# Kernel optimization log

Measured on AMD Instinct MI355X. Metric: run time of the kernel, lower is better.

The kernel has to match this reference:

```python
import jax, jax.numpy as jnp
import numpy as np

N, Fdim, Aout = 8192, 32, 8
AVG_DEG = 32.0  # target average degree for the random graph


def setup_inputs() -> dict:
    key = jax.random.key(0)
    ks = jax.random.split(key, 12)
    x = jax.random.normal(ks[0], (N, Fdim), dtype=jnp.float32)
    # binary adjacency, zero diagonal (GCNConv adds self-loops itself)
    u = jax.random.uniform(ks[1], (N, N), dtype=jnp.float32)
    adj = (u < (AVG_DEG / N)).astype(jnp.float32)
    adj = adj * (1.0 - jnp.eye(N, dtype=jnp.float32))
    mask = (jax.random.uniform(ks[2], (N,), dtype=jnp.float32) < 0.5).astype(jnp.float32)

    def lin(k, fout, fin):
        s = 1.0 / np.sqrt(fin)
        return jax.random.uniform(k, (fout, fin), jnp.float32, -s, s)

    return {
        "x": x, "adj": adj, "mask": mask,
        "w1": lin(ks[3], 64, Fdim), "b1": jnp.zeros((64,), jnp.float32),
        "w2": lin(ks[4], 128, 64), "b2": jnp.zeros((128,), jnp.float32),
        "wg": lin(ks[5], 128, 128), "bg": jnp.zeros((128,), jnp.float32),
        "wd": lin(ks[6], 128, 128), "bd": jnp.zeros((128,), jnp.float32),
        "wp1": lin(ks[7], 128, 256), "bp1": jnp.zeros((128,), jnp.float32),
        "wp2": lin(ks[8], 64, 128), "bp2": jnp.zeros((64,), jnp.float32),
        "wo": lin(ks[9], Aout, 64), "bo": jnp.zeros((Aout,), jnp.float32),
    }


def reference(x, adj, mask, w1, b1, w2, b2, wg, bg, wd, bd, wp1, bp1, wp2, bp2, wo, bo):
    # encoder MLP
    h = jax.nn.relu(x @ w1.T + b1)           # [N,64]
    h = jax.nn.relu(h @ w2.T + b2)           # [N,128]
    # GCNConv with default self-loops and symmetric normalization:
    # out = D^{-1/2} (A + I) D^{-1/2} (h W^T) + b
    a_hat = adj + jnp.eye(adj.shape[0], dtype=adj.dtype)
    deg = jnp.sum(a_hat, axis=1)             # >= 1 thanks to self-loops
    dinv = jax.lax.rsqrt(deg)
    msg = h @ wg.T                            # [N,128]
    agg = dinv[:, None] * (a_hat @ (dinv[:, None] * msg))  # normalized aggregation
    g = jax.nn.relu(agg + bg)
    g = jax.nn.relu(g @ wd.T + bd)
    f = jnp.concatenate([g, h], axis=1)       # [N,256]
    p = jax.nn.relu(f @ wp1.T + bp1)
    p = jax.nn.relu(p @ wp2.T + bp2)
    out = (p @ wo.T + bo) * mask[:, None]     # [N,Aout]
    return out
```

## Files before the change

kernel.cpp:

```cpp
#include <hip/hip_runtime.h>

#define N_NODES 8192
#define CAP 128
constexpr int AST = 132;

typedef unsigned u32x4 __attribute__((ext_vector_type(4)));
typedef unsigned short u16;
typedef __attribute__((ext_vector_type(8))) short bf16x8;
typedef __attribute__((ext_vector_type(4))) float f32x4;

constexpr size_t OFF_WD  = 0;
constexpr size_t OFF_WP1 = 16384;
constexpr size_t OFF_WP2 = 49152;
constexpr size_t OFF_WO  = 57344;
constexpr size_t OFF_W1  = 58368;
constexpr size_t OFF_W2  = 60416;
constexpr size_t OFF_WG  = 68608;
constexpr size_t WTOT    = 84992;

__global__ __launch_bounds__(256, 4) void scan_kernel(
    const float* __restrict__ adj, int* __restrict__ cnt,
    int* __restrict__ nbr) {
  const int t = threadIdx.x;
  const int lane = t & 63;
  const int row = blockIdx.x * 4 + (t >> 6);
  const u32x4* rowp = (const u32x4*)(adj + (size_t)row * N_NODES);
  u32x4 v[8], vn[8];
#pragma unroll
  for (int i = 0; i < 8; ++i) v[i] = __builtin_nontemporal_load(&rowp[i * 64 + lane]);
  int running = 0;
  int* nbr_row = nbr + (size_t)row * CAP;
  for (int ch = 0; ch < 4; ++ch) {
    if (ch < 3) {
      const u32x4* cp = rowp + (ch + 1) * 512;
#pragma unroll
      for (int i = 0; i < 8; ++i) vn[i] = __builtin_nontemporal_load(&cp[i * 64 + lane]);
    }
    int c = 0;
#pragma unroll
    for (int i = 0; i < 8; ++i)
      c += (v[i].x != 0u) + (v[i].y != 0u) + (v[i].z != 0u) + (v[i].w != 0u);
    int incl = c;
#pragma unroll
    for (int s = 1; s < 64; s <<= 1) {
      int n = __shfl_up(incl, s);
      if (lane >= s) incl += n;
    }
    int off = running + incl - c;
    running += __shfl(incl, 63);
    const int colbase = ch * 2048;
#pragma unroll
    for (int i = 0; i < 8; ++i) {
      if (v[i].x | v[i].y | v[i].z | v[i].w) {
        const int col = colbase + (i * 64 + lane) * 4;
        if (v[i].x) { if (off < CAP) nbr_row[off] = col + 0; ++off; }
        if (v[i].y) { if (off < CAP) nbr_row[off] = col + 1; ++off; }
        if (v[i].z) { if (off < CAP) nbr_row[off] = col + 2; ++off; }
        if (v[i].w) { if (off < CAP) nbr_row[off] = col + 3; ++off; }
      }
    }
#pragma unroll
    for (int i = 0; i < 8; ++i) v[i] = vn[i];
  }
  if (lane == 0) cnt[row] = running;
}

__global__ __launch_bounds__(256) void agg_kernel(
    const int* __restrict__ cnt, const int* __restrict__ nbr,
    const float* __restrict__ msg, const float* __restrict__ bg,
    const float* __restrict__ adj, float* __restrict__ g1) {
  const int t = threadIdx.x;
  const int f = t & 127;
  const int rA = blockIdx.x * 4 + (t >> 7) * 2;
  const int rB = rA + 1;
  const int cA = cnt[rA], cB = cnt[rB];
  float a0 = msg[(size_t)rA * 128 + f];
  float a1 = msg[(size_t)rB * 128 + f];
  if (cA <= CAP && cB <= CAP) {
    const int* nA = nbr + (size_t)rA * CAP;
    const int* nB = nbr + (size_t)rB * CAP;
    const int cm = max(cA, cB);
    for (int i = 0; i < cm; i += 4) {
#pragma unroll
      for (int k = 0; k < 4; ++k) {
        const int ii = i + k;
        int jA = nA[ii < cA ? ii : 0] & (N_NODES - 1);
        int jB = nB[ii < cB ? ii : 0] & (N_NODES - 1);
        float vA = msg[(size_t)jA * 128 + f];
        float vB = msg[(size_t)jB * 128 + f];
        a0 += (ii < cA) ? vA : 0.f;
        a1 += (ii < cB) ? vB : 0.f;
      }
    }
  } else {
    a0 = msg[(size_t)rA * 128 + f];
    a1 = msg[(size_t)rB * 128 + f];
    for (int col = 0; col < N_NODES; ++col) {
      if (adj[(size_t)rA * N_NODES + col] != 0.f) a0 += msg[(size_t)col * 128 + f];
      if (adj[(size_t)rB * N_NODES + col] != 0.f) a1 += msg[(size_t)col * 128 + f];
    }
  }
  float o0 = fmaf(rsqrtf((float)cA + 1.0f), a0, bg[f]);
  float o1 = fmaf(rsqrtf((float)cB + 1.0f), a1, bg[f]);
  g1[(size_t)rA * 128 + f] = fmaxf(o0, 0.f);
  g1[(size_t)rB * 128 + f] = fmaxf(o1, 0.f);
}

__global__ __launch_bounds__(256) void prep_weights(
    const float* __restrict__ wd, const float* __restrict__ wp1,
    const float* __restrict__ wp2, const float* __restrict__ wo,
    const float* __restrict__ w1, const float* __restrict__ w2,
    const float* __restrict__ wg,
    u16* __restrict__ bh, u16* __restrict__ bl) {
  const int gid = blockIdx.x * 256 + threadIdx.x;
  if (gid >= (int)WTOT) return;
  const float* W; int K, F; size_t off; int rel; bool pad = false;
  if (gid < 16384)      { W = wd;  K = 128; F = 128; off = OFF_WD;  rel = gid; }
  else if (gid < 49152) { W = wp1; K = 256; F = 128; off = OFF_WP1; rel = gid - 16384; }
  else if (gid < 57344) { W = wp2; K = 128; F = 64;  off = OFF_WP2; rel = gid - 49152; }
  else if (gid < 58368) { W = wo;  K = 64;  F = 16;  off = OFF_WO;  rel = gid - 57344; pad = true; }
  else if (gid < 60416) { W = w1;  K = 32;  F = 64;  off = OFF_W1;  rel = gid - 58368; }
  else if (gid < 68608) { W = w2;  K = 64;  F = 128; off = OFF_W2;  rel = gid - 60416; }
  else                  { W = wg;  K = 128; F = 128; off = OFF_WG;  rel = gid - 68608; }
  const int j = rel & 7, lane = (rel >> 3) & 63, t2 = rel >> 9;
  const int nf = F >> 4;
  const int ftile = t2 % nf, kstep = t2 / nf;
  const int k = kstep * 32 + ((lane >> 4) << 3) + j;
  const int f = ftile * 16 + (lane & 15);
  const float v = (pad && f >= 8) ? 0.f : W[(size_t)f * K + k];
  const unsigned u = __float_as_uint(v);
  const unsigned uh = u & 0xffff0000u;
  const float r = v - __uint_as_float(uh);
  bh[off + rel] = (u16)(uh >> 16);
  bl[off + rel] = (u16)(__float_as_uint(r) >> 16);
}

template <int K, int F, int KSPLIT, int SA, int SO, bool RELU, bool BIAS, int SCALEMODE>
__device__ __forceinline__ void mfma_layer(
    const float (*__restrict__ A0)[SA], const float (*__restrict__ A1)[SA],
    const u16* __restrict__ Bh, const u16* __restrict__ Bl,
    const float* __restrict__ bias, float (*__restrict__ O)[SO],
    float* __restrict__ gout, int gstride,
    const float* __restrict__ mask, const int* __restrict__ cntp,
    int nbase, int lane) {
  constexpr int NK = K / 32, NF = F / 16;
  f32x4 acc[NF];
  const f32x4 zz = {0.f, 0.f, 0.f, 0.f};
#pragma unroll
  for (int i = 0; i < NF; ++i) acc[i] = zz;
  const int arow = lane & 15;
  const int kgrp = (lane >> 4) << 3;
#pragma unroll
  for (int ks = 0; ks < NK; ++ks) {
    const float* ap = (ks * 32 < KSPLIT) ? &A0[arow][ks * 32 + kgrp]
                                         : &A1[arow][ks * 32 - KSPLIT + kgrp];
    const float4 p0 = *(const float4*)ap;
    const float4 p1 = *(const float4*)(ap + 4);
    const float av[8] = {p0.x, p0.y, p0.z, p0.w, p1.x, p1.y, p1.z, p1.w};
    bf16x8 ahi, alo;
#pragma unroll
    for (int j = 0; j < 8; ++j) {
      const unsigned u = __float_as_uint(av[j]);
      const unsigned uh = u & 0xffff0000u;
      const float r = av[j] - __uint_as_float(uh);
      ahi[j] = (short)(uh >> 16);
      alo[j] = (short)(__float_as_uint(r) >> 16);
    }
#pragma unroll
    for (int ft = 0; ft < NF; ++ft) {
      const size_t idx = ((size_t)(ks * NF + ft) * 64 + lane) * 8;
      const bf16x8 wh = *(const bf16x8*)(Bh + idx);
      const bf16x8 wl = *(const bf16x8*)(Bl + idx);
      acc[ft] = __builtin_amdgcn_mfma_f32_16x16x32_bf16(ahi, wh, acc[ft], 0, 0, 0);
      acc[ft] = __builtin_amdgcn_mfma_f32_16x16x32_bf16(ahi, wl, acc[ft], 0, 0, 0);
      acc[ft] = __builtin_amdgcn_mfma_f32_16x16x32_bf16(alo, wh, acc[ft], 0, 0, 0);
    }
  }
#pragma unroll
  for (int ft = 0; ft < NF; ++ft) {
    const int f = ft * 16 + (lane & 15);
    if (SCALEMODE == 1 && F == 16 && f >= 8) continue;
    const float bv = BIAS ? bias[f] : 0.f;
#pragma unroll
    for (int r = 0; r < 4; ++r) {
      const int row = ((lane >> 4) << 2) + r;
      const int node = nbase + row;
      float v = acc[ft][r];
      if (BIAS) v += bv;
      if (RELU) v = fmaxf(v, 0.f);
      if (SCALEMODE == 1) v *= mask[node];
      if (SCALEMODE == 2) v *= rsqrtf((float)cntp[node] + 1.0f);
      if (O) O[row][f] = v;
      if (gout) gout[(size_t)node * gstride + f] = v;
    }
  }
}

__global__ __launch_bounds__(128) void mfma_encode(
    const float* __restrict__ x, const u16* __restrict__ bh,
    const u16* __restrict__ bl, const float* __restrict__ b1,
    const float* __restrict__ b2, const int* __restrict__ cnt,
    float* __restrict__ h_out, float* __restrict__ msg_out) {
  __shared__ float actX[2][16][36];
  __shared__ float actH1[2][16][68];
  __shared__ float actH[2][16][AST];
  const int t = threadIdx.x;
  const int w = t >> 6, lane = t & 63;
  const int n0 = blockIdx.x * 32 + w * 16;
#pragma unroll
  for (int i = 0; i < 2; ++i) {
    const int fi = i * 64 + lane;
    const int row = fi >> 3, c4 = (fi & 7) * 4;
    *(float4*)&actX[w][row][c4] = *(const float4*)&x[(size_t)(n0 + row) * 32 + c4];
  }
  __syncthreads();
  mfma_layer<32, 64, 32, 36, 68, true, true, 0>(
      actX[w], actX[w], bh + OFF_W1, bl + OFF_W1, b1, actH1[w],
      nullptr, 0, nullptr, nullptr, n0, lane);
  __syncthreads();
  mfma_layer<64, 128, 64, 68, AST, true, true, 0>(
      actH1[w], actH1[w], bh + OFF_W2, bl + OFF_W2, b2, actH[w],
      h_out, 128, nullptr, nullptr, n0, lane);
  __syncthreads();
  mfma_layer<128, 128, 128, AST, AST, false, false, 2>(
      actH[w], actH[w], bh + OFF_WG, bl + OFF_WG, nullptr, (float(*)[AST])nullptr,
      msg_out, 128, nullptr, cnt, n0, lane);
}

__global__ __launch_bounds__(128) void mfma_decode(
    const float* __restrict__ g1, const float* __restrict__ h,
    const u16* __restrict__ bh, const u16* __restrict__ bl,
    const float* __restrict__ bd, const float* __restrict__ bp1,
    const float* __restrict__ bp2, const float* __restrict__ bo,
    const float* __restrict__ mask, float* __restrict__ out) {
  __shared__ float actA[2][16][AST];
  __shared__ float actB[2][16][AST];
  __shared__ float actH[2][16][AST];
  const int t = threadIdx.x;
  const int w = t >> 6, lane = t & 63;
  const int n0 = blockIdx.x * 32 + w * 16;
#pragma unroll
  for (int i = 0; i < 8; ++i) {
    const int fi = i * 64 + lane;
    const int row = fi >> 5, c4 = (fi & 31) * 4;
    *(float4*)&actA[w][row][c4] = *(const float4*)&g1[(size_t)(n0 + row) * 128 + c4];
    *(float4*)&actH[w][row][c4] = *(const float4*)&h[(size_t)(n0 + row) * 128 + c4];
  }
  __syncthreads();
  mfma_layer<128, 128, 128, AST, AST, true, true, 0>(
      actA[w], actA[w], bh + OFF_WD, bl + OFF_WD, bd, actB[w],
      nullptr, 0, nullptr, nullptr, n0, lane);
  __syncthreads();
  mfma_layer<256, 128, 128, AST, AST, true, true, 0>(
      actB[w], actH[w], bh + OFF_WP1, bl + OFF_WP1, bp1, actA[w],
      nullptr, 0, nullptr, nullptr, n0, lane);
  __syncthreads();
  mfma_layer<128, 64, 128, AST, AST, true, true, 0>(
      actA[w], actA[w], bh + OFF_WP2, bl + OFF_WP2, bp2, actB[w],
      nullptr, 0, nullptr, nullptr, n0, lane);
  __syncthreads();
  mfma_layer<64, 16, 128, AST, AST, false, true, 1>(
      actB[w], actB[w], bh + OFF_WO, bl + OFF_WO, bo, (float(*)[AST])nullptr,
      out, 8, mask, nullptr, n0, lane);
}

extern "C" void kernel_launch(void* const* d_in, const int* in_sizes, int n_in,
                              void* d_out, int out_size, void* d_ws, size_t ws_size,
                              hipStream_t stream) {
  const float* x    = (const float*)d_in[0];
  const float* adj  = (const float*)d_in[1];
  const float* mask = (const float*)d_in[2];
  const float* w1   = (const float*)d_in[3];
  const float* b1   = (const float*)d_in[4];
  const float* w2   = (const float*)d_in[5];
  const float* b2   = (const float*)d_in[6];
  const float* wg   = (const float*)d_in[7];
  const float* bg   = (const float*)d_in[8];
  const float* wd   = (const float*)d_in[9];
  const float* bd   = (const float*)d_in[10];
  const float* wp1  = (const float*)d_in[11];
  const float* bp1  = (const float*)d_in[12];
  const float* wp2  = (const float*)d_in[13];
  const float* bp2  = (const float*)d_in[14];
  const float* wo   = (const float*)d_in[15];
  const float* bo   = (const float*)d_in[16];
  float* out = (float*)d_out;

  float* ws = (float*)d_ws;
  float* h    = ws; ws += (size_t)N_NODES * 128;
  float* msg  = ws; ws += (size_t)N_NODES * 128;
  float* g1   = ws; ws += (size_t)N_NODES * 128;
  int* cnt = (int*)ws; ws += N_NODES;
  int* nbr = (int*)ws; ws += (size_t)N_NODES * CAP;
  u16* bh = (u16*)ws;
  u16* bl = bh + WTOT;

  prep_weights<<<(int)((WTOT + 255) / 256), 256, 0, stream>>>(
      wd, wp1, wp2, wo, w1, w2, wg, bh, bl);
  scan_kernel<<<N_NODES / 4, 256, 0, stream>>>(adj, cnt, nbr);
  mfma_encode<<<N_NODES / 32, 128, 0, stream>>>(x, bh, bl, b1, b2, cnt, h, msg);
  agg_kernel<<<N_NODES / 4, 256, 0, stream>>>(cnt, nbr, msg, bg, adj, g1);
  mfma_decode<<<N_NODES / 32, 128, 0, stream>>>(g1, h, bh, bl, bd, bp1, bp2, bo, mask, out);
}
```

Baseline: 430.6 us.

## Fuse weight prep, adjacency scan and encoder into one block-specialized kernel

```diff
diff --git a/kernel.cpp b/kernel.cpp
--- a/kernel.cpp
+++ b/kernel.cpp
@@ -13,136 +13,22 @@
 constexpr size_t OFF_WP1 = 16384;
 constexpr size_t OFF_WP2 = 49152;
 constexpr size_t OFF_WO  = 57344;
-constexpr size_t OFF_W1  = 58368;
-constexpr size_t OFF_W2  = 60416;
-constexpr size_t OFF_WG  = 68608;
-constexpr size_t WTOT    = 84992;
-
-__global__ __launch_bounds__(256, 4) void scan_kernel(
-    const float* __restrict__ adj, int* __restrict__ cnt,
-    int* __restrict__ nbr) {
-  const int t = threadIdx.x;
-  const int lane = t & 63;
-  const int row = blockIdx.x * 4 + (t >> 6);
-  const u32x4* rowp = (const u32x4*)(adj + (size_t)row * N_NODES);
-  u32x4 v[8], vn[8];
-#pragma unroll
-  for (int i = 0; i < 8; ++i) v[i] = __builtin_nontemporal_load(&rowp[i * 64 + lane]);
-  int running = 0;
-  int* nbr_row = nbr + (size_t)row * CAP;
-  for (int ch = 0; ch < 4; ++ch) {
-    if (ch < 3) {
-      const u32x4* cp = rowp + (ch + 1) * 512;
-#pragma unroll
-      for (int i = 0; i < 8; ++i) vn[i] = __builtin_nontemporal_load(&cp[i * 64 + lane]);
-    }
-    int c = 0;
-#pragma unroll
-    for (int i = 0; i < 8; ++i)
-      c += (v[i].x != 0u) + (v[i].y != 0u) + (v[i].z != 0u) + (v[i].w != 0u);
-    int incl = c;
-#pragma unroll
-    for (int s = 1; s < 64; s <<= 1) {
-      int n = __shfl_up(incl, s);
-      if (lane >= s) incl += n;
-    }
-    int off = running + incl - c;
-    running += __shfl(incl, 63);
-    const int colbase = ch * 2048;
-#pragma unroll
-    for (int i = 0; i < 8; ++i) {
-      if (v[i].x | v[i].y | v[i].z | v[i].w) {
-        const int col = colbase + (i * 64 + lane) * 4;
-        if (v[i].x) { if (off < CAP) nbr_row[off] = col + 0; ++off; }
-        if (v[i].y) { if (off < CAP) nbr_row[off] = col + 1; ++off; }
-        if (v[i].z) { if (off < CAP) nbr_row[off] = col + 2; ++off; }
-        if (v[i].w) { if (off < CAP) nbr_row[off] = col + 3; ++off; }
-      }
-    }
-#pragma unroll
-    for (int i = 0; i < 8; ++i) v[i] = vn[i];
-  }
-  if (lane == 0) cnt[row] = running;
-}
-
-__global__ __launch_bounds__(256) void agg_kernel(
-    const int* __restrict__ cnt, const int* __restrict__ nbr,
-    const float* __restrict__ msg, const float* __restrict__ bg,
-    const float* __restrict__ adj, float* __restrict__ g1) {
-  const int t = threadIdx.x;
-  const int f = t & 127;
-  const int rA = blockIdx.x * 4 + (t >> 7) * 2;
-  const int rB = rA + 1;
-  const int cA = cnt[rA], cB = cnt[rB];
-  float a0 = msg[(size_t)rA * 128 + f];
-  float a1 = msg[(size_t)rB * 128 + f];
-  if (cA <= CAP && cB <= CAP) {
-    const int* nA = nbr + (size_t)rA * CAP;
-    const int* nB = nbr + (size_t)rB * CAP;
-    const int cm = max(cA, cB);
-    for (int i = 0; i < cm; i += 4) {
-#pragma unroll
-      for (int k = 0; k < 4; ++k) {
-        const int ii = i + k;
-        int jA = nA[ii < cA ? ii : 0] & (N_NODES - 1);
-        int jB = nB[ii < cB ? ii : 0] & (N_NODES - 1);
-        float vA = msg[(size_t)jA * 128 + f];
-        float vB = msg[(size_t)jB * 128 + f];
-        a0 += (ii < cA) ? vA : 0.f;
-        a1 += (ii < cB) ? vB : 0.f;
-      }
-    }
-  } else {
-    a0 = msg[(size_t)rA * 128 + f];
-    a1 = msg[(size_t)rB * 128 + f];
-    for (int col = 0; col < N_NODES; ++col) {
-      if (adj[(size_t)rA * N_NODES + col] != 0.f) a0 += msg[(size_t)col * 128 + f];
-      if (adj[(size_t)rB * N_NODES + col] != 0.f) a1 += msg[(size_t)col * 128 + f];
-    }
-  }
-  float o0 = fmaf(rsqrtf((float)cA + 1.0f), a0, bg[f]);
-  float o1 = fmaf(rsqrtf((float)cB + 1.0f), a1, bg[f]);
-  g1[(size_t)rA * 128 + f] = fmaxf(o0, 0.f);
-  g1[(size_t)rB * 128 + f] = fmaxf(o1, 0.f);
-}
-
-__global__ __launch_bounds__(256) void prep_weights(
-    const float* __restrict__ wd, const float* __restrict__ wp1,
-    const float* __restrict__ wp2, const float* __restrict__ wo,
-    const float* __restrict__ w1, const float* __restrict__ w2,
-    const float* __restrict__ wg,
-    u16* __restrict__ bh, u16* __restrict__ bl) {
-  const int gid = blockIdx.x * 256 + threadIdx.x;
-  if (gid >= (int)WTOT) return;
-  const float* W; int K, F; size_t off; int rel; bool pad = false;
-  if (gid < 16384)      { W = wd;  K = 128; F = 128; off = OFF_WD;  rel = gid; }
-  else if (gid < 49152) { W = wp1; K = 256; F = 128; off = OFF_WP1; rel = gid - 16384; }
-  else if (gid < 57344) { W = wp2; K = 128; F = 64;  off = OFF_WP2; rel = gid - 49152; }
-  else if (gid < 58368) { W = wo;  K = 64;  F = 16;  off = OFF_WO;  rel = gid - 57344; pad = true; }
-  else if (gid < 60416) { W = w1;  K = 32;  F = 64;  off = OFF_W1;  rel = gid - 58368; }
-  else if (gid < 68608) { W = w2;  K = 64;  F = 128; off = OFF_W2;  rel = gid - 60416; }
-  else                  { W = wg;  K = 128; F = 128; off = OFF_WG;  rel = gid - 68608; }
-  const int j = rel & 7, lane = (rel >> 3) & 63, t2 = rel >> 9;
-  const int nf = F >> 4;
-  const int ftile = t2 % nf, kstep = t2 / nf;
-  const int k = kstep * 32 + ((lane >> 4) << 3) + j;
-  const int f = ftile * 16 + (lane & 15);
-  const float v = (pad && f >= 8) ? 0.f : W[(size_t)f * K + k];
-  const unsigned u = __float_as_uint(v);
-  const unsigned uh = u & 0xffff0000u;
-  const float r = v - __uint_as_float(uh);
-  bh[off + rel] = (u16)(uh >> 16);
-  bl[off + rel] = (u16)(__float_as_uint(r) >> 16);
-}
-
-template <int K, int F, int KSPLIT, int SA, int SO, bool RELU, bool BIAS, int SCALEMODE>
+constexpr size_t WTOT    = 58368;
+
+#define ENC_BLOCKS 128
+#define SCAN_BLOCKS 2048
+#define PREP_BLOCKS 228
+#define FUSED_GRID (ENC_BLOCKS + SCAN_BLOCKS + PREP_BLOCKS)
+
+template <int K, int F, int KSPLIT, int SA, int SO, bool RELU, bool BIAS,
+          int SCALEMODE, bool RAWB>
 __device__ __forceinline__ void mfma_layer(
     const float (*__restrict__ A0)[SA], const float (*__restrict__ A1)[SA],
     const u16* __restrict__ Bh, const u16* __restrict__ Bl,
+    const float* __restrict__ Wraw,
     const float* __restrict__ bias, float (*__restrict__ O)[SO],
     float* __restrict__ gout, int gstride,
-    const float* __restrict__ mask, const int* __restrict__ cntp,
-    int nbase, int lane) {
+    const float* __restrict__ mask, int nbase, int lane) {
   constexpr int NK = K / 32, NF = F / 16;
   f32x4 acc[NF];
   const f32x4 zz = {0.f, 0.f, 0.f, 0.f};
@@ -168,9 +54,25 @@
     }
 #pragma unroll
     for (int ft = 0; ft < NF; ++ft) {
-      const size_t idx = ((size_t)(ks * NF + ft) * 64 + lane) * 8;
-      const bf16x8 wh = *(const bf16x8*)(Bh + idx);
-      const bf16x8 wl = *(const bf16x8*)(Bl + idx);
+      bf16x8 wh, wl;
+      if (RAWB) {
+        const float* wp = Wraw + (size_t)(ft * 16 + arow) * K + ks * 32 + kgrp;
+        const float4 q0 = *(const float4*)wp;
+        const float4 q1 = *(const float4*)(wp + 4);
+        const float wv[8] = {q0.x, q0.y, q0.z, q0.w, q1.x, q1.y, q1.z, q1.w};
+#pragma unroll
+        for (int j = 0; j < 8; ++j) {
+          const unsigned u = __float_as_uint(wv[j]);
+          const unsigned uh = u & 0xffff0000u;
+          const float r = wv[j] - __uint_as_float(uh);
+          wh[j] = (short)(uh >> 16);
+          wl[j] = (short)(__float_as_uint(r) >> 16);
+        }
+      } else {
+        const size_t idx = ((size_t)(ks * NF + ft) * 64 + lane) * 8;
+        wh = *(const bf16x8*)(Bh + idx);
+        wl = *(const bf16x8*)(Bl + idx);
+      }
       acc[ft] = __builtin_amdgcn_mfma_f32_16x16x32_bf16(ahi, wh, acc[ft], 0, 0, 0);
       acc[ft] = __builtin_amdgcn_mfma_f32_16x16x32_bf16(ahi, wl, acc[ft], 0, 0, 0);
       acc[ft] = __builtin_amdgcn_mfma_f32_16x16x32_bf16(alo, wh, acc[ft], 0, 0, 0);
@@ -189,42 +91,156 @@
       if (BIAS) v += bv;
       if (RELU) v = fmaxf(v, 0.f);
       if (SCALEMODE == 1) v *= mask[node];
-      if (SCALEMODE == 2) v *= rsqrtf((float)cntp[node] + 1.0f);
       if (O) O[row][f] = v;
       if (gout) gout[(size_t)node * gstride + f] = v;
     }
   }
 }
 
-__global__ __launch_bounds__(128) void mfma_encode(
-    const float* __restrict__ x, const u16* __restrict__ bh,
-    const u16* __restrict__ bl, const float* __restrict__ b1,
-    const float* __restrict__ b2, const int* __restrict__ cnt,
-    float* __restrict__ h_out, float* __restrict__ msg_out) {
-  __shared__ float actX[2][16][36];
-  __shared__ float actH1[2][16][68];
-  __shared__ float actH[2][16][AST];
+__global__ __launch_bounds__(256, 2) void fused_sep_kernel(
+    const float* __restrict__ adj, const float* __restrict__ x,
+    const float* __restrict__ w1, const float* __restrict__ b1,
+    const float* __restrict__ w2, const float* __restrict__ b2,
+    const float* __restrict__ wg,
+    const float* __restrict__ wd, const float* __restrict__ wp1,
+    const float* __restrict__ wp2, const float* __restrict__ wo,
+    int* __restrict__ cnt, float* __restrict__ dinv, int* __restrict__ nbr,
+    float* __restrict__ h_out, float* __restrict__ msg_out,
+    u16* __restrict__ bh, u16* __restrict__ bl) {
+  __shared__ float actX[4][16][36];
+  __shared__ float actH1[4][16][68];
+  __shared__ float actH[4][16][AST];
   const int t = threadIdx.x;
-  const int w = t >> 6, lane = t & 63;
-  const int n0 = blockIdx.x * 32 + w * 16;
-#pragma unroll
-  for (int i = 0; i < 2; ++i) {
-    const int fi = i * 64 + lane;
-    const int row = fi >> 3, c4 = (fi & 7) * 4;
-    *(float4*)&actX[w][row][c4] = *(const float4*)&x[(size_t)(n0 + row) * 32 + c4];
-  }
-  __syncthreads();
-  mfma_layer<32, 64, 32, 36, 68, true, true, 0>(
-      actX[w], actX[w], bh + OFF_W1, bl + OFF_W1, b1, actH1[w],
-      nullptr, 0, nullptr, nullptr, n0, lane);
-  __syncthreads();
-  mfma_layer<64, 128, 64, 68, AST, true, true, 0>(
-      actH1[w], actH1[w], bh + OFF_W2, bl + OFF_W2, b2, actH[w],
-      h_out, 128, nullptr, nullptr, n0, lane);
-  __syncthreads();
-  mfma_layer<128, 128, 128, AST, AST, false, false, 2>(
-      actH[w], actH[w], bh + OFF_WG, bl + OFF_WG, nullptr, (float(*)[AST])nullptr,
-      msg_out, 128, nullptr, cnt, n0, lane);
+  const int bid = blockIdx.x;
+
+  if (bid < ENC_BLOCKS) {
+    const int w = t >> 6, lane = t & 63;
+    const int n0 = bid * 64 + w * 16;
+#pragma unroll
+    for (int i = 0; i < 2; ++i) {
+      const int fi = i * 256 + t;
+      const int row = fi >> 3, c4 = (fi & 7) * 4;
+      *(float4*)&actX[0][0][(size_t)row * 36 + c4] =
+          *(const float4*)&x[(size_t)(bid * 64 + row) * 32 + c4];
+    }
+    __syncthreads();
+    mfma_layer<32, 64, 32, 36, 68, true, true, 0, true>(
+        actX[w], actX[w], nullptr, nullptr, w1, b1, actH1[w],
+        nullptr, 0, nullptr, n0, lane);
+    __syncthreads();
+    mfma_layer<64, 128, 64, 68, AST, true, true, 0, true>(
+        actH1[w], actH1[w], nullptr, nullptr, w2, b2, actH[w],
+        h_out, 128, nullptr, n0, lane);
+    __syncthreads();
+    mfma_layer<128, 128, 128, AST, AST, false, false, 0, true>(
+        actH[w], actH[w], nullptr, nullptr, wg, nullptr, (float(*)[AST])nullptr,
+        msg_out, 128, nullptr, n0, lane);
+  } else if (bid < ENC_BLOCKS + SCAN_BLOCKS) {
+    const int lane = t & 63;
+    const int row = (bid - ENC_BLOCKS) * 4 + (t >> 6);
+    const u32x4* rowp = (const u32x4*)(adj + (size_t)row * N_NODES);
+    u32x4 v[8], vn[8];
+#pragma unroll
+    for (int i = 0; i < 8; ++i) v[i] = __builtin_nontemporal_load(&rowp[i * 64 + lane]);
+    int running = 0;
+    int* nbr_row = nbr + (size_t)row * CAP;
+    for (int ch = 0; ch < 4; ++ch) {
+      if (ch < 3) {
+        const u32x4* cp = rowp + (ch + 1) * 512;
+#pragma unroll
+        for (int i = 0; i < 8; ++i) vn[i] = __builtin_nontemporal_load(&cp[i * 64 + lane]);
+      }
+      int c = 0;
+#pragma unroll
+      for (int i = 0; i < 8; ++i)
+        c += (v[i].x != 0u) + (v[i].y != 0u) + (v[i].z != 0u) + (v[i].w != 0u);
+      int incl = c;
+#pragma unroll
+      for (int s = 1; s < 64; s <<= 1) {
+        int n = __shfl_up(incl, s);
+        if (lane >= s) incl += n;
+      }
+      int off = running + incl - c;
+      running += __shfl(incl, 63);
+      const int colbase = ch * 2048;
+#pragma unroll
+      for (int i = 0; i < 8; ++i) {
+        if (v[i].x | v[i].y | v[i].z | v[i].w) {
+          const int col = colbase + (i * 64 + lane) * 4;
+          if (v[i].x) { if (off < CAP) nbr_row[off] = col + 0; ++off; }
+          if (v[i].y) { if (off < CAP) nbr_row[off] = col + 1; ++off; }
+          if (v[i].z) { if (off < CAP) nbr_row[off] = col + 2; ++off; }
+          if (v[i].w) { if (off < CAP) nbr_row[off] = col + 3; ++off; }
+        }
+      }
+#pragma unroll
+      for (int i = 0; i < 8; ++i) v[i] = vn[i];
+    }
+    if (lane == 0) {
+      cnt[row] = running;
+      dinv[row] = rsqrtf((float)running + 1.0f);
+    }
+  } else {
+    const int gid = (bid - ENC_BLOCKS - SCAN_BLOCKS) * 256 + t;
+    if (gid >= (int)WTOT) return;
+    const float* W; int K, F; size_t off; int rel; bool pad = false;
+    if (gid < 16384)      { W = wd;  K = 128; F = 128; off = OFF_WD;  rel = gid; }
+    else if (gid < 49152) { W = wp1; K = 256; F = 128; off = OFF_WP1; rel = gid - 16384; }
+    else if (gid < 57344) { W = wp2; K = 128; F = 64;  off = OFF_WP2; rel = gid - 49152; }
+    else                  { W = wo;  K = 64;  F = 16;  off = OFF_WO;  rel = gid - 57344; pad = true; }
+    const int j = rel & 7, lane8 = (rel >> 3) & 63, t2 = rel >> 9;
+    const int nf = F >> 4;
+    const int ftile = t2 % nf, kstep = t2 / nf;
+    const int k = kstep * 32 + ((lane8 >> 4) << 3) + j;
+    const int f = ftile * 16 + (lane8 & 15);
+    const float v = (pad && f >= 8) ? 0.f : W[(size_t)f * K + k];
+    const unsigned u = __float_as_uint(v);
+    const unsigned uh = u & 0xffff0000u;
+    const float r = v - __uint_as_float(uh);
+    bh[off + rel] = (u16)(uh >> 16);
+    bl[off + rel] = (u16)(__float_as_uint(r) >> 16);
+  }
+}
+
+__global__ __launch_bounds__(256) void agg_kernel(
+    const int* __restrict__ cnt, const float* __restrict__ dinv,
+    const int* __restrict__ nbr, const float* __restrict__ msg,
+    const float* __restrict__ bg, const float* __restrict__ adj,
+    float* __restrict__ g1) {
+  const int t = threadIdx.x;
+  const int f = t & 127;
+  const int rA = blockIdx.x * 4 + (t >> 7) * 2;
+  const int rB = rA + 1;
+  const int cA = cnt[rA], cB = cnt[rB];
+  const float dvA = dinv[rA], dvB = dinv[rB];
+  float a0 = dvA * msg[(size_t)rA * 128 + f];
+  float a1 = dvB * msg[(size_t)rB * 128 + f];
+  if (cA <= CAP && cB <= CAP) {
+    const int* nA = nbr + (size_t)rA * CAP;
+    const int* nB = nbr + (size_t)rB * CAP;
+    const int cm = max(cA, cB);
+    for (int i = 0; i < cm; i += 4) {
+#pragma unroll
+      for (int k = 0; k < 4; ++k) {
+        const int ii = i + k;
+        int jA = nA[ii < cA ? ii : 0] & (N_NODES - 1);
+        int jB = nB[ii < cB ? ii : 0] & (N_NODES - 1);
+        const float wA = (ii < cA) ? dinv[jA] : 0.f;
+        const float wB = (ii < cB) ? dinv[jB] : 0.f;
+        a0 = fmaf(wA, msg[(size_t)jA * 128 + f], a0);
+        a1 = fmaf(wB, msg[(size_t)jB * 128 + f], a1);
+      }
+    }
+  } else {
+    for (int col = 0; col < N_NODES; ++col) {
+      if (adj[(size_t)rA * N_NODES + col] != 0.f)
+        a0 = fmaf(dinv[col], msg[(size_t)col * 128 + f], a0);
+      if (adj[(size_t)rB * N_NODES + col] != 0.f)
+        a1 = fmaf(dinv[col], msg[(size_t)col * 128 + f], a1);
+    }
+  }
+  g1[(size_t)rA * 128 + f] = fmaxf(fmaf(dvA, a0, bg[f]), 0.f);
+  g1[(size_t)rB * 128 + f] = fmaxf(fmaf(dvB, a1, bg[f]), 0.f);
 }
 
 __global__ __launch_bounds__(128) void mfma_decode(
@@ -247,21 +263,21 @@
     *(float4*)&actH[w][row][c4] = *(const float4*)&h[(size_t)(n0 + row) * 128 + c4];
   }
   __syncthreads();
-  mfma_layer<128, 128, 128, AST, AST, true, true, 0>(
-      actA[w], actA[w], bh + OFF_WD, bl + OFF_WD, bd, actB[w],
-      nullptr, 0, nullptr, nullptr, n0, lane);
+  mfma_layer<128, 128, 128, AST, AST, true, true, 0, false>(
+      actA[w], actA[w], bh + OFF_WD, bl + OFF_WD, nullptr, bd, actB[w],
+      nullptr, 0, nullptr, n0, lane);
   __syncthreads();
-  mfma_layer<256, 128, 128, AST, AST, true, true, 0>(
-      actB[w], actH[w], bh + OFF_WP1, bl + OFF_WP1, bp1, actA[w],
-      nullptr, 0, nullptr, nullptr, n0, lane);
+  mfma_layer<256, 128, 128, AST, AST, true, true, 0, false>(
+      actB[w], actH[w], bh + OFF_WP1, bl + OFF_WP1, nullptr, bp1, actA[w],
+      nullptr, 0, nullptr, n0, lane);
   __syncthreads();
-  mfma_layer<128, 64, 128, AST, AST, true, true, 0>(
-      actA[w], actA[w], bh + OFF_WP2, bl + OFF_WP2, bp2, actB[w],
-      nullptr, 0, nullptr, nullptr, n0, lane);
+  mfma_layer<128, 64, 128, AST, AST, true, true, 0, false>(
+      actA[w], actA[w], bh + OFF_WP2, bl + OFF_WP2, nullptr, bp2, actB[w],
+      nullptr, 0, nullptr, n0, lane);
   __syncthreads();
-  mfma_layer<64, 16, 128, AST, AST, false, true, 1>(
-      actB[w], actB[w], bh + OFF_WO, bl + OFF_WO, bo, (float(*)[AST])nullptr,
-      out, 8, mask, nullptr, n0, lane);
+  mfma_layer<64, 16, 128, AST, AST, false, true, 1, false>(
+      actB[w], actB[w], bh + OFF_WO, bl + OFF_WO, nullptr, bo,
+      (float(*)[AST])nullptr, out, 8, mask, n0, lane);
 }
 
 extern "C" void kernel_launch(void* const* d_in, const int* in_sizes, int n_in,
@@ -290,15 +306,16 @@
   float* h    = ws; ws += (size_t)N_NODES * 128;
   float* msg  = ws; ws += (size_t)N_NODES * 128;
   float* g1   = ws; ws += (size_t)N_NODES * 128;
+  float* dinv = ws; ws += N_NODES;
   int* cnt = (int*)ws; ws += N_NODES;
   int* nbr = (int*)ws; ws += (size_t)N_NODES * CAP;
   u16* bh = (u16*)ws;
   u16* bl = bh + WTOT;
 
-  prep_weights<<<(int)((WTOT + 255) / 256), 256, 0, stream>>>(
-      wd, wp1, wp2, wo, w1, w2, wg, bh, bl);
-  scan_kernel<<<N_NODES / 4, 256, 0, stream>>>(adj, cnt, nbr);
-  mfma_encode<<<N_NODES / 32, 128, 0, stream>>>(x, bh, bl, b1, b2, cnt, h, msg);
-  agg_kernel<<<N_NODES / 4, 256, 0, stream>>>(cnt, nbr, msg, bg, adj, g1);
-  mfma_decode<<<N_NODES / 32, 128, 0, stream>>>(g1, h, bh, bl, bd, bp1, bp2, bo, mask, out);
-}
+  fused_sep_kernel<<<FUSED_GRID, 256, 0, stream>>>(
+      adj, x, w1, b1, w2, b2, wg, wd, wp1, wp2, wo,
+      cnt, dinv, nbr, h, msg, bh, bl);
+  agg_kernel<<<N_NODES / 4, 256, 0, stream>>>(cnt, dinv, nbr, msg, bg, adj, g1);
+  mfma_decode<<<N_NODES / 32, 128, 0, stream>>>(
+      g1, h, bh, bl, bd, bp1, bp2, bo, mask, out);
+}
```

Result: no change. 433.6 us (+0.7%).
